# Performance work log

Hardware: AMD Instinct MI355X
Metric: run time of the kernel (lower is better)

The kernel has to match this reference:

```python
import jax, jax.numpy as jnp
import numpy as np
import math

DIM = 1024
HEADS = 16
SEQ_LEN = 2048
NUM_PV = 32
HEAD_DIM = DIM // HEADS
EPS = 1e-5


def setup_inputs() -> dict:
    key = jax.random.key(0)
    k1, k2 = jax.random.split(key)
    B = 4
    L = SEQ_LEN + NUM_PV
    x = jax.random.normal(k1, (B, L, DIM), dtype=jnp.float32)
    paramvecs = jax.random.normal(k2, (1, NUM_PV, DIM), dtype=jnp.float32)
    return {"x": x, "paramvecs": paramvecs}


def _layernorm_noaffine(x):
    mu = jnp.mean(x, axis=-1, keepdims=True)
    var = jnp.mean(jnp.square(x - mu), axis=-1, keepdims=True)
    return (x - mu) * jax.lax.rsqrt(var + EPS)


def reference(x, paramvecs):
    B, L, D = x.shape  # L = SEQ_LEN + NUM_PV
    # add learned param vectors onto the trailing num_paramvec positions
    x = x.at[:, SEQ_LEN:, :].add(paramvecs)
    residual = x
    xn = _layernorm_noaffine(x)
    # shared Q = K = V = xn, split into heads: [B, H, L, Dh]
    h = xn.reshape(B, L, HEADS, HEAD_DIM).transpose(0, 2, 1, 3)
    scores = jnp.einsum('bhqd,bhkd->bhqk', h, h) / math.sqrt(HEAD_DIM)
    weights = jax.nn.softmax(scores, axis=-1)
    context = jnp.einsum('bhqk,bhkd->bhqd', weights, h)
    context = context.transpose(0, 2, 1, 3).reshape(B, L, D)
    return context + residual
```

## Files before the change

### kernel.cpp

```cpp
#include <hip/hip_runtime.h>
#include <hip/hip_fp16.h>

#define DIMF 1024
#define NHEADS 16
#define SEQ 2048
#define NPV 32
#define HD 64
#define LTOT 2080
#define LP 2112
#define NB 4
#define BHN 64
#define NQT 33
#define QB 128
#define NQB 17
#define NKV 65

typedef _Float16 f16x8 __attribute__((ext_vector_type(8)));
typedef float f32x16 __attribute__((ext_vector_type(16)));
typedef unsigned short u16x8 __attribute__((ext_vector_type(8)));
typedef int v2i __attribute__((ext_vector_type(2)));

#if __has_builtin(__builtin_amdgcn_exp2f)
#define EXP2(x) __builtin_amdgcn_exp2f(x)
#else
#define EXP2(x) exp2f(x)
#endif

#define CEXP 0.1803368801111f
#define KSH  11.5415603271f

__global__ __launch_bounds__(256) void prep_kernel(const float* __restrict__ x,
                                                   const float* __restrict__ pv,
                                                   unsigned short* __restrict__ xnh) {
  int row = blockIdx.x;
  int b = row / LP, l = row - b * LP;
  int t = threadIdx.x;
  int h = t >> 4;
  int dd = (t & 15) << 2;
  unsigned short* dst = xnh + ((size_t)(b * NHEADS + h) * LP + l) * HD + dd;
  if (l >= LTOT) {
    *reinterpret_cast<ushort4*>(dst) = make_ushort4(0, 0, 0, 0);
    return;
  }
  const float* xr = x + ((size_t)b * LTOT + l) * DIMF + t * 4;
  float4 v = *reinterpret_cast<const float4*>(xr);
  if (l >= SEQ) {
    float4 p = *reinterpret_cast<const float4*>(pv + (size_t)(l - SEQ) * DIMF + t * 4);
    v.x += p.x; v.y += p.y; v.z += p.z; v.w += p.w;
  }

  float s1 = v.x + v.y + v.z + v.w;
  float s2 = v.x * v.x + v.y * v.y + v.z * v.z + v.w * v.w;
#pragma unroll
  for (int o = 1; o < 64; o <<= 1) { s1 += __shfl_xor(s1, o); s2 += __shfl_xor(s2, o); }
  __shared__ float red[8];
  int wv = t >> 6;
  if ((t & 63) == 0) { red[wv] = s1; red[4 + wv] = s2; }
  __syncthreads();
  s1 = red[0] + red[1] + red[2] + red[3];
  s2 = red[4] + red[5] + red[6] + red[7];
  float mu = s1 * (1.0f / DIMF);
  float var = s2 * (1.0f / DIMF) - mu * mu;
  float rs = rsqrtf(var + 1e-5f);
  ushort4 o4;
  o4.x = __half_as_ushort(__float2half((v.x - mu) * rs));
  o4.y = __half_as_ushort(__float2half((v.y - mu) * rs));
  o4.z = __half_as_ushort(__float2half((v.z - mu) * rs));
  o4.w = __half_as_ushort(__float2half((v.w - mu) * rs));
  *reinterpret_cast<ushort4*>(dst) = o4;
}

__global__ __launch_bounds__(256) void transpose_kernel(const unsigned short* __restrict__ xnh,
                                                        unsigned short* __restrict__ xnt) {
  __shared__ unsigned short tile[64][72];
  int blk = blockIdx.x;
  int bh = blk / NQT, lt = blk - bh * NQT;
  int t = threadIdx.x;
  int rr = t >> 3;
  int c8 = (t & 7) << 3;
#pragma unroll
  for (int p = 0; p < 2; p++) {
    int ll = rr + p * 32;
    float4 v = *reinterpret_cast<const float4*>(xnh + ((size_t)bh * LP + lt * 64 + ll) * HD + c8);
    int cs = c8 ^ (((ll >> 3) & 7) << 3);
    *reinterpret_cast<float4*>(&tile[ll][cs]) = v;
  }
  __syncthreads();
  int l8 = (t & 7) << 3;
#pragma unroll
  for (int p = 0; p < 2; p++) {
    int d = rr + p * 32;
    u16x8 o;
#pragma unroll
    for (int j = 0; j < 8; j++) {
      o[j] = tile[l8 + j][d ^ ((t & 7) << 3)];
    }
    *reinterpret_cast<u16x8*>(xnt + ((size_t)bh * HD + d) * LP + lt * 64 + l8) = o;
  }
}

static __device__ __forceinline__ f32x16 mfma32(f16x8 a, f16x8 b, f32x16 c) {
  return __builtin_amdgcn_mfma_f32_32x32x16_f16(a, b, c, 0, 0, 0);
}

static __device__ __forceinline__ unsigned cvtpk(float a, float b) {
  auto h = __builtin_amdgcn_cvt_pkrtz(a, b);
  return __builtin_bit_cast(unsigned, h);
}

static __device__ __forceinline__ void pack2(const f32x16& P, f16x8& f0, f16x8& f1) {
  unsigned a0 = cvtpk(P[0], P[1]),  b0 = cvtpk(P[4], P[5]);
  unsigned a1 = cvtpk(P[2], P[3]),  b1 = cvtpk(P[6], P[7]);
  v2i s0 = __builtin_amdgcn_permlane32_swap(a0, b0, false, false);
  v2i s1 = __builtin_amdgcn_permlane32_swap(a1, b1, false, false);
  unsigned a2 = cvtpk(P[8], P[9]),   b2 = cvtpk(P[12], P[13]);
  unsigned a3 = cvtpk(P[10], P[11]), b3 = cvtpk(P[14], P[15]);
  v2i s2 = __builtin_amdgcn_permlane32_swap(a2, b2, false, false);
  v2i s3 = __builtin_amdgcn_permlane32_swap(a3, b3, false, false);
  union { unsigned u[4]; f16x8 v; } u0, u1;
  u0.u[0] = (unsigned)s0.x; u0.u[1] = (unsigned)s1.x; u0.u[2] = (unsigned)s0.y; u0.u[3] = (unsigned)s1.y;
  u1.u[0] = (unsigned)s2.x; u1.u[1] = (unsigned)s3.x; u1.u[2] = (unsigned)s2.y; u1.u[3] = (unsigned)s3.y;
  f0 = u0.v; f1 = u1.v;
}

#define GLDS(src, dst) \
  __builtin_amdgcn_global_load_lds( \
      (const __attribute__((address_space(1))) unsigned int*)(src), \
      (__attribute__((address_space(3))) unsigned int*)(dst), 16, 0, 0)

__device__ __forceinline__ void kv_step16(const unsigned short* kbuf, const unsigned short* vbuf,
                                          const f16x8 (&qf)[4], const f32x16& kshC,
                                          const f16x8& onesv,
                                          f32x16& accA, f32x16& accB, f32x16& accS,
                                          int l31, int hi, int sw) {
  const unsigned short* k0 = kbuf + (size_t)l31 * 64;
  f32x16 st;
  __builtin_amdgcn_s_setprio(1);
#pragma unroll
  for (int ds = 0; ds < 4; ds++) {
    int cl = ds * 2 + hi;
    f16x8 ka = *reinterpret_cast<const f16x8*>(k0 + ((cl ^ sw) << 3));
    st = mfma32(ka, qf[ds], ds == 0 ? kshC : st);
  }
  __builtin_amdgcn_s_setprio(0);
#pragma unroll
  for (int r = 0; r < 16; r++) st[r] = EXP2(st[r]);
  f16x8 pa[2];
  pack2(st, pa[0], pa[1]);
  const unsigned short* v0 = vbuf + (size_t)l31 * 64;
  __builtin_amdgcn_s_setprio(1);
  accS = mfma32(pa[0], onesv, accS);
  accS = mfma32(pa[1], onesv, accS);
#pragma unroll
  for (int ks = 0; ks < 2; ks++) {
    int clA = ks * 2 + hi;
    f16x8 bvA = *reinterpret_cast<const f16x8*>(v0 + ((clA ^ sw) << 3));
    accA = mfma32(pa[ks], bvA, accA);
    int clB = 4 + ks * 2 + hi;
    f16x8 bvB = *reinterpret_cast<const f16x8*>(v0 + ((clB ^ sw) << 3));
    accB = mfma32(pa[ks], bvB, accB);
  }
  __builtin_amdgcn_s_setprio(0);
}

__global__ __launch_bounds__(256, 2) void attn_kernel(const unsigned short* __restrict__ xnh,
                                                      const unsigned short* __restrict__ xnt,
                                                      const float* __restrict__ x,
                                                      const float* __restrict__ pvin,
                                                      float* __restrict__ out) {
  __shared__ unsigned short kA[2 * 2048], kB[2 * 2048];
  __shared__ unsigned short vA[2 * 2048], vB[2 * 2048];
  int bid = blockIdx.x;
  const int nwg = BHN * NQB;
  const int cpx = nwg >> 3;
  int wg = (bid & 7) * cpx + (bid >> 3);
  int bh = wg / NQB, qt = wg - bh * NQB;
  int b = bh >> 4, h = bh & 15;
  int tid = threadIdx.x;
  int wid = tid >> 6;
  int lane = tid & 63;
  int l31 = lane & 31, hi = lane >> 5;
  int sw = l31 & 7;
  int q0w = qt * QB + wid * 32;
  const unsigned short* Kb = xnh + (size_t)bh * (LP * HD);
  const unsigned short* Vb = xnt + (size_t)bh * (HD * LP);

  f16x8 qf[4];
  const _Float16 ce = (_Float16)CEXP;
  const f16x8 cev = {ce, ce, ce, ce, ce, ce, ce, ce};
#pragma unroll
  for (int ds = 0; ds < 4; ds++) {
    qf[ds] = *reinterpret_cast<const f16x8*>(Kb + (size_t)(q0w + l31) * HD + ds * 16 + hi * 8);
    qf[ds] = qf[ds] * cev;
  }
  f32x16 kshC;
#pragma unroll
  for (int r = 0; r < 16; r++) kshC[r] = -KSH;
  const _Float16 one = (_Float16)1.0f;
  const f16x8 onesv = {one, one, one, one, one, one, one, one};

  f32x16 accA = {};
  f32x16 accB = {};
  f32x16 accS = {};

  int r = tid >> 3, cp = tid & 7;
  int cl = cp ^ (r & 7);
  const unsigned short* pK = Kb + (size_t)r * HD + cl * 8;
  const unsigned short* pV = Vb + (size_t)(r + 32 * (cl >> 2)) * LP + (cl & 3) * 8;
  int wo = wid * 512;

#define STAGEP(kb, vb) do { \
    GLDS(pK, (kb) + wo); GLDS(pK + 2048, (kb) + 2048 + wo); \
    GLDS(pV, (vb) + wo); GLDS(pV + 32, (vb) + 2048 + wo); \
    pK += 4096; pV += 64; } while (0)

  STAGEP(kA, vA);
  __syncthreads();

  for (int it = 0; it < 16; ++it) {
    STAGEP(kB, vB);
    kv_step16(kA,        vA,        qf, kshC, onesv, accA, accB, accS, l31, hi, sw);
    kv_step16(kA + 2048, vA + 2048, qf, kshC, onesv, accA, accB, accS, l31, hi, sw);
    __syncthreads();
    STAGEP(kA, vA);
    kv_step16(kB,        vB,        qf, kshC, onesv, accA, accB, accS, l31, hi, sw);
    kv_step16(kB + 2048, vB + 2048, qf, kshC, onesv, accA, accB, accS, l31, hi, sw);
    __syncthreads();
  }
  kv_step16(kA, vA, qf, kshC, onesv, accA, accB, accS, l31, hi, sw);

  const float* xbase = x + (size_t)b * LTOT * DIMF + h * HD + l31;
  float* obase = out + (size_t)b * LTOT * DIMF + h * HD + l31;
  const float* pvbase = pvin + (size_t)h * HD + l31;
  if (q0w < LTOT) {
#pragma unroll
    for (int q2 = 0; q2 < 4; q2++) {
#pragma unroll
      for (int j = 0; j < 4; j++) {
        int rr = q2 * 4 + j;
        int qg = q0w + q2 * 8 + hi * 4 + j;
        float ivj = 1.0f / accS[rr];
        const float* xp = xbase + (size_t)qg * DIMF;
        float r0 = xp[0], r1 = xp[32];
        if (qg >= SEQ) {
          const float* pp = pvbase + (size_t)(qg - SEQ) * DIMF;
          r0 += pp[0]; r1 += pp[32];
        }
        float* p = obase + (size_t)qg * DIMF;
        p[0]  = r0 + accA[rr] * ivj;
        p[32] = r1 + accB[rr] * ivj;
      }
    }
  }
#undef STAGEP
}

extern "C" void kernel_launch(void* const* d_in, const int* in_sizes, int n_in,
                              void* d_out, int out_size, void* d_ws, size_t ws_size,
                              hipStream_t stream) {
  const float* x  = (const float*)d_in[0];
  const float* pv = (const float*)d_in[1];
  float* out = (float*)d_out;
  unsigned short* xnh = (unsigned short*)d_ws;
  unsigned short* xnt = xnh + (size_t)BHN * LP * HD;
  prep_kernel<<<NB * LP, 256, 0, stream>>>(x, pv, xnh);
  transpose_kernel<<<BHN * NQT, 256, 0, stream>>>(xnh, xnt);
  attn_kernel<<<BHN * NQB, 256, 0, stream>>>(xnh, xnt, x, pv, out);
}
```

Before: 117.4 us.

## Load K/V fragments directly from global memory instead of LDS staging

Removes the double-buffered shared-memory staging of K and V tiles (global_load_lds plus barriers) and has each wave read its K and V fragments directly from global memory every KV step. This drops LDS traffic and block-wide synchronisation, and could raise occupancy since no LDS is used. In exchange the four waves of a block each re-read the same K/V data from global/L2, with no explicit prefetch, so load latency may be exposed to the MFMA loop.

```diff
diff --git a/kernel.cpp b/kernel.cpp
--- a/kernel.cpp
+++ b/kernel.cpp
@@ -123,23 +123,17 @@
   f0 = u0.v; f1 = u1.v;
 }
 
-#define GLDS(src, dst) \
-  __builtin_amdgcn_global_load_lds( \
-      (const __attribute__((address_space(1))) unsigned int*)(src), \
-      (__attribute__((address_space(3))) unsigned int*)(dst), 16, 0, 0)
-
-__device__ __forceinline__ void kv_step16(const unsigned short* kbuf, const unsigned short* vbuf,
-                                          const f16x8 (&qf)[4], const f32x16& kshC,
-                                          const f16x8& onesv,
-                                          f32x16& accA, f32x16& accB, f32x16& accS,
-                                          int l31, int hi, int sw) {
-  const unsigned short* k0 = kbuf + (size_t)l31 * 64;
+__device__ __forceinline__ void kv_step_direct(const unsigned short* __restrict__ krow,
+                                               const unsigned short* __restrict__ va,
+                                               const unsigned short* __restrict__ vb,
+                                               const f16x8 (&qf)[4], const f32x16& kshC,
+                                               const f16x8& onesv,
+                                               f32x16& accA, f32x16& accB, f32x16& accS) {
   f32x16 st;
   __builtin_amdgcn_s_setprio(1);
 #pragma unroll
   for (int ds = 0; ds < 4; ds++) {
-    int cl = ds * 2 + hi;
-    f16x8 ka = *reinterpret_cast<const f16x8*>(k0 + ((cl ^ sw) << 3));
+    f16x8 ka = *reinterpret_cast<const f16x8*>(krow + ds * 16);
     st = mfma32(ka, qf[ds], ds == 0 ? kshC : st);
   }
   __builtin_amdgcn_s_setprio(0);
@@ -147,17 +141,14 @@
   for (int r = 0; r < 16; r++) st[r] = EXP2(st[r]);
   f16x8 pa[2];
   pack2(st, pa[0], pa[1]);
-  const unsigned short* v0 = vbuf + (size_t)l31 * 64;
   __builtin_amdgcn_s_setprio(1);
   accS = mfma32(pa[0], onesv, accS);
   accS = mfma32(pa[1], onesv, accS);
 #pragma unroll
   for (int ks = 0; ks < 2; ks++) {
-    int clA = ks * 2 + hi;
-    f16x8 bvA = *reinterpret_cast<const f16x8*>(v0 + ((clA ^ sw) << 3));
+    f16x8 bvA = *reinterpret_cast<const f16x8*>(va + ks * 16);
     accA = mfma32(pa[ks], bvA, accA);
-    int clB = 4 + ks * 2 + hi;
-    f16x8 bvB = *reinterpret_cast<const f16x8*>(v0 + ((clB ^ sw) << 3));
+    f16x8 bvB = *reinterpret_cast<const f16x8*>(vb + ks * 16);
     accB = mfma32(pa[ks], bvB, accB);
   }
   __builtin_amdgcn_s_setprio(0);
@@ -168,8 +159,6 @@
                                                       const float* __restrict__ x,
                                                       const float* __restrict__ pvin,
                                                       float* __restrict__ out) {
-  __shared__ unsigned short kA[2 * 2048], kB[2 * 2048];
-  __shared__ unsigned short vA[2 * 2048], vB[2 * 2048];
   int bid = blockIdx.x;
   const int nwg = BHN * NQB;
   const int cpx = nwg >> 3;
@@ -180,7 +169,6 @@
   int wid = tid >> 6;
   int lane = tid & 63;
   int l31 = lane & 31, hi = lane >> 5;
-  int sw = l31 & 7;
   int q0w = qt * QB + wid * 32;
   const unsigned short* Kb = xnh + (size_t)bh * (LP * HD);
   const unsigned short* Vb = xnt + (size_t)bh * (HD * LP);
@@ -203,31 +191,15 @@
   f32x16 accB = {};
   f32x16 accS = {};
 
-  int r = tid >> 3, cp = tid & 7;
-  int cl = cp ^ (r & 7);
-  const unsigned short* pK = Kb + (size_t)r * HD + cl * 8;
-  const unsigned short* pV = Vb + (size_t)(r + 32 * (cl >> 2)) * LP + (cl & 3) * 8;
-  int wo = wid * 512;
-
-#define STAGEP(kb, vb) do { \
-    GLDS(pK, (kb) + wo); GLDS(pK + 2048, (kb) + 2048 + wo); \
-    GLDS(pV, (vb) + wo); GLDS(pV + 32, (vb) + 2048 + wo); \
-    pK += 4096; pV += 64; } while (0)
-
-  STAGEP(kA, vA);
-  __syncthreads();
-
-  for (int it = 0; it < 16; ++it) {
-    STAGEP(kB, vB);
-    kv_step16(kA,        vA,        qf, kshC, onesv, accA, accB, accS, l31, hi, sw);
-    kv_step16(kA + 2048, vA + 2048, qf, kshC, onesv, accA, accB, accS, l31, hi, sw);
-    __syncthreads();
-    STAGEP(kA, vA);
-    kv_step16(kB,        vB,        qf, kshC, onesv, accA, accB, accS, l31, hi, sw);
-    kv_step16(kB + 2048, vB + 2048, qf, kshC, onesv, accA, accB, accS, l31, hi, sw);
-    __syncthreads();
-  }
-  kv_step16(kA, vA, qf, kshC, onesv, accA, accB, accS, l31, hi, sw);
+  const unsigned short* krow = Kb + (size_t)l31 * HD + hi * 8;
+  const unsigned short* va = Vb + (size_t)l31 * LP + hi * 8;
+  const unsigned short* vb = va + (size_t)32 * LP;
+
+#pragma unroll 2
+  for (int t = 0; t < NKV; ++t) {
+    kv_step_direct(krow, va, vb, qf, kshC, onesv, accA, accB, accS);
+    krow += 32 * HD; va += 32; vb += 32;
+  }
 
   const float* xbase = x + (size_t)b * LTOT * DIMF + h * HD + l31;
   float* obase = out + (size_t)b * LTOT * DIMF + h * HD + l31;
@@ -252,7 +224,6 @@
       }
     }
   }
-#undef STAGEP
 }
 
 extern "C" void kernel_launch(void* const* d_in, const int* in_sizes, int n_in,
```

New measurement: 352.6 us. +200.2%, slower.
